# Performance work log

Measured on AMD Instinct MI355X. Metric: run time of the kernel, lower is better.

The kernel has to match this reference:

```python
import jax, jax.numpy as jnp
import numpy as np
import math

B, S, D, H = 4, 1024, 1024, 16
DK = D // H


def setup_inputs() -> dict:
    key = jax.random.key(0)
    ks = jax.random.split(key, 13)
    s = 1.0 / math.sqrt(D)
    inp = {
        "query": jax.random.normal(ks[0], (B, S, D), jnp.float32),
        "key": jax.random.normal(ks[1], (B, S, D), jnp.float32),
        "value": jax.random.normal(ks[2], (B, S, D), jnp.float32),
        "mask": jax.random.randint(ks[3], (B, S, S), 0, 2, jnp.int32),
        "wq": jax.random.normal(ks[4], (D, D), jnp.float32) * s,
        "bq": jax.random.normal(ks[5], (D,), jnp.float32) * s,
        "wk": jax.random.normal(ks[6], (D, D), jnp.float32) * s,
        "bk": jax.random.normal(ks[7], (D,), jnp.float32) * s,
        "wv": jax.random.normal(ks[8], (D, D), jnp.float32) * s,
        "bv": jax.random.normal(ks[9], (D,), jnp.float32) * s,
        "wo": jax.random.normal(ks[10], (D, D), jnp.float32) * s,
        "bo": jax.random.normal(ks[11], (D,), jnp.float32) * s,
    }
    return inp


def reference(query, key, value, mask, wq, bq, wk, bk, wv, bv, wo, bo):
    # QKV projections, split into heads: [B,S,D] -> [B,H,S,DK]
    def proj(x, w, b):
        return (x @ w.T + b).reshape(B, S, H, DK).transpose(0, 2, 1, 3)

    q = proj(query, wq, bq)
    k = proj(key, wk, bk)
    v = proj(value, wv, bv)

    scores = jnp.einsum("bhqd,bhkd->bhqk", q, k) / math.sqrt(DK)
    scores = scores + mask[:, None, :, :].astype(scores.dtype) * (-1e9)
    p = jax.nn.softmax(scores, axis=-1)
    x = jnp.einsum("bhqk,bhkd->bhqd", p, v)
    x = x.transpose(0, 2, 1, 3).reshape(B, S, D)
    # output projection (dropout is identity in eval)
    return x @ wo.T + bo
```

## Files before the change

### kernel.cpp

```cpp
#include <hip/hip_runtime.h>
#include <hip/hip_bf16.h>


typedef __bf16 bf16x8 __attribute__((ext_vector_type(8)));
typedef float f32x4 __attribute__((ext_vector_type(4)));
typedef unsigned short us8 __attribute__((ext_vector_type(8)));
typedef unsigned short us4 __attribute__((ext_vector_type(4)));

#define MFMA(a, b, c) __builtin_amdgcn_mfma_f32_16x16x32_bf16(a, b, c, 0, 0, 0)
#define EXP2(x) __builtin_amdgcn_exp2f(x)

__device__ __forceinline__ unsigned short f2b(float f) {
  return __builtin_bit_cast(unsigned short, __float2bfloat16(f));
}
__device__ __forceinline__ float b2f(unsigned short u) {
  return __builtin_bit_cast(float, (unsigned)u << 16);
}
__device__ __forceinline__ unsigned cvtpk(float lo, float hi) {
  unsigned r;
  asm("v_cvt_pk_bf16_f32 %0, %1, %2" : "=v"(r) : "v"(lo), "v"(hi));
  return r;
}
__device__ __forceinline__ bf16x8 ldbf8(const unsigned short* p) {
  return __builtin_bit_cast(bf16x8, *reinterpret_cast<const us8*>(p));
}
__device__ __forceinline__ us8 cvt8(float4 a, float4 b) {
  us8 o;
  o[0] = f2b(a.x); o[1] = f2b(a.y); o[2] = f2b(a.z); o[3] = f2b(a.w);
  o[4] = f2b(b.x); o[5] = f2b(b.y); o[6] = f2b(b.z); o[7] = f2b(b.w);
  return o;
}
__device__ __forceinline__ void glds16(const void* g, void* l) {
  __builtin_amdgcn_global_load_lds(
      (const __attribute__((address_space(1))) unsigned int*)g,
      (__attribute__((address_space(3))) unsigned int*)l, 16, 0, 0);
}

__global__ __launch_bounds__(256)
void prep(const float* __restrict__ query, const float* __restrict__ key,
          const float* __restrict__ value, const float* __restrict__ wq,
          const float* __restrict__ wk, const float* __restrict__ wv,
          unsigned short* __restrict__ Abfq, unsigned short* __restrict__ Abfk,
          unsigned short* __restrict__ Abfv, unsigned short* __restrict__ Wb) {
  const int bid = blockIdx.x, tid = threadIdx.x;
  const float* src;
  unsigned short* dst;
  size_t off;
  if (bid < 1536) {
    const int widx = bid >> 9;
    src = (widx == 0) ? wq : (widx == 1) ? wk : wv;
    dst = Wb + (size_t)widx * 1048576;
    off = (size_t)(bid & 511) * 2048 + tid * 8;
  } else if (bid < 3584) {
    src = query; dst = Abfq; off = (size_t)(bid - 1536) * 2048 + tid * 8;
  } else if (bid < 5632) {
    src = key; dst = Abfk; off = (size_t)(bid - 3584) * 2048 + tid * 8;
  } else {
    src = value; dst = Abfv; off = (size_t)(bid - 5632) * 2048 + tid * 8;
  }
  const float4* p = reinterpret_cast<const float4*>(src + off);
  *reinterpret_cast<us8*>(dst + off) = cvt8(p[0], p[1]);
}

__global__ __launch_bounds__(256)
void maskcvt(const int* __restrict__ mask, unsigned short* __restrict__ Mf) {
  const int idx = blockIdx.x * 256 + threadIdx.x;
  const int wl = idx & 63, tile = idx >> 6;
  const int kt = tile & 63, qt = (tile >> 6) & 63, b = tile >> 12;
  const int lr = wl & 15, lg = wl >> 4;
  const int4 mv = *reinterpret_cast<const int4*>(
      mask + (size_t)(b * 1024 + qt * 16 + lr) * 1024 + kt * 16 + lg * 4);
  us4 o;
  o[0] = mv.x ? 0xCEACu : 0xC1C0u;
  o[1] = mv.y ? 0xCEACu : 0xC1C0u;
  o[2] = mv.z ? 0xCEACu : 0xC1C0u;
  o[3] = mv.w ? 0xCEACu : 0xC1C0u;
  *reinterpret_cast<us4*>(Mf + (size_t)idx * 4) = o;
}

__global__ __launch_bounds__(256)
void cvt_w(const float* __restrict__ src, unsigned short* __restrict__ dst) {
  const size_t off = (size_t)blockIdx.x * 2048 + threadIdx.x * 8;
  const float4* p = reinterpret_cast<const float4*>(src + off);
  *reinterpret_cast<us8*>(dst + off) = cvt8(p[0], p[1]);
}

__global__ __launch_bounds__(256, 4)
void gemm_proj(const unsigned short* __restrict__ Aq,
               const unsigned short* __restrict__ Ak,
               const unsigned short* __restrict__ Av_bf,
               const float* __restrict__ Av_f32,
               const unsigned short* __restrict__ Wb,
               const float* __restrict__ bq, const float* __restrict__ bk,
               const float* __restrict__ bv, unsigned short* __restrict__ Qb,
               unsigned short* __restrict__ Kf, unsigned short* __restrict__ Vf,
               float qscale) {
  constexpr int K = 1024, N = 1024;
  __shared__ __align__(16) unsigned short As[2][128 * 32];
  __shared__ __align__(16) unsigned short Bs[2][128 * 32];
  const int lid = blockIdx.x + (blockIdx.y << 5) + (blockIdx.z << 8);
  const int xcd = lid & 7, slot = lid >> 3;
  const int chunk = ((slot >> 3) << 3) + xcd;
  const int z = chunk >> 5;
  const int bm = (chunk & 31) * 128;
  const int bn = (slot & 7) * 128;

  const unsigned short* Abf = (z == 0) ? Aq : (z == 1) ? Ak : Av_bf;
  const bool f32path = (z == 2) && (Av_bf == nullptr);
  const unsigned short* Bw = Wb + (size_t)z * 1048576;
  const float* bias = (z == 0) ? bq : (z == 1) ? bk : bv;
  const int t = threadIdx.x;
  const int w = t >> 6, lane = t & 63, lr = lane & 15, lg = lane >> 4;
  const int wr = w >> 1, wc = w & 1;

#define SWZ(row) ((((row) ^ ((row) >> 2)) & 3) << 4)

  f32x4 acc[4][4];
#pragma unroll
  for (int m = 0; m < 4; ++m)
#pragma unroll
    for (int n = 0; n < 4; ++n) acc[m][n] = f32x4{0.f, 0.f, 0.f, 0.f};

  auto stageA = [&](int k0, int buf) {
#pragma unroll
    for (int it = 0; it < 2; ++it) {
      const int s = it * 256 + t, row = s >> 2, cb = (s & 3) * 16;
      const char* g = (const char*)Abf + ((size_t)(bm + row) * 1024 + k0) * 2 +
                      (cb ^ SWZ(row));
      char* l = (char*)&As[buf][0] + (it * 256 + w * 64) * 16;
      glds16(g, l);
    }
  };
  auto stageB = [&](int k0, int buf) {
#pragma unroll
    for (int it = 0; it < 2; ++it) {
      const int s = it * 256 + t, row = s >> 2, cb = (s & 3) * 16;
      const char* g = (const char*)Bw + ((size_t)(bn + row) * 1024 + k0) * 2 +
                      (cb ^ SWZ(row));
      char* l = (char*)&Bs[buf][0] + (it * 256 + w * 64) * 16;
      glds16(g, l);
    }
  };
#define STA8(buf, it, v)                                                       \
  {                                                                            \
    const int s_ = (it) * 256 + t, row_ = s_ >> 2, cb_ = (s_ & 3) * 16;        \
    *reinterpret_cast<us8*>((char*)&As[buf][0] + row_ * 64 +                   \
                            (cb_ ^ SWZ(row_))) = (v);                          \
  }

  if (f32path) {
#pragma unroll
    for (int it = 0; it < 2; ++it) {
      const int s = it * 256 + t, row = s >> 2, col = (s & 3) * 8;
      const float4* p =
          reinterpret_cast<const float4*>(Av_f32 + (size_t)(bm + row) * K + col);
      STA8(0, it, cvt8(p[0], p[1]));
    }
  } else {
    stageA(0, 0);
  }
  stageB(0, 0);
  __syncthreads();

  for (int c = 0; c < 32; ++c) {
    const int buf = c & 1;
    float4 fa[4];
    if (c < 31) {
      const int k1 = (c + 1) * 32;
      if (f32path) {
#pragma unroll
        for (int it = 0; it < 2; ++it) {
          const int s = it * 256 + t, row = s >> 2, col = (s & 3) * 8;
          const float4* p = reinterpret_cast<const float4*>(
              Av_f32 + (size_t)(bm + row) * K + k1 + col);
          fa[2 * it] = p[0];
          fa[2 * it + 1] = p[1];
        }
      } else {
        stageA(k1, buf ^ 1);
      }
      stageB(k1, buf ^ 1);
    }
    {
      bf16x8 af[4], bfr[4];
#pragma unroll
      for (int m = 0; m < 4; ++m) {
        const int row = wr * 64 + m * 16 + lr;
        af[m] = ldbf8((const unsigned short*)((char*)&As[buf][0] + row * 64 +
                                              ((lg * 16) ^ SWZ(row))));
      }
#pragma unroll
      for (int n = 0; n < 4; ++n) {
        const int row = wc * 64 + n * 16 + lr;
        bfr[n] = ldbf8((const unsigned short*)((char*)&Bs[buf][0] + row * 64 +
                                               ((lg * 16) ^ SWZ(row))));
      }
#pragma unroll
      for (int m = 0; m < 4; ++m)
#pragma unroll
        for (int n = 0; n < 4; ++n) acc[m][n] = MFMA(af[m], bfr[n], acc[m][n]);
    }
    if (c < 31 && f32path) {
#pragma unroll
      for (int it = 0; it < 2; ++it) STA8(buf ^ 1, it, cvt8(fa[2 * it], fa[2 * it + 1]));
    }
    __syncthreads();
  }
#undef STA8
#undef SWZ

#pragma unroll
  for (int m = 0; m < 4; ++m) {
    const int mr = bm + wr * 64 + m * 16 + lg * 4;
#pragma unroll
    for (int nt = 0; nt < 4; ++nt) {
      const int n = bn + wc * 64 + nt * 16 + lr;
      const float bb = bias[n];
      if (z == 0) {
#pragma unroll
        for (int r = 0; r < 4; ++r)
          Qb[(size_t)(mr + r) * N + n] = f2b((acc[m][nt][r] + bb) * qscale);
      } else if (z == 1) {
        const int b2 = mr >> 10, s0 = mr & 1023, hh = n >> 6, dd = n & 63;
        const size_t base = (size_t)(b2 * 16 + hh) * 65536 + (size_t)(dd >> 5) * 32768 +
                            (size_t)(s0 >> 4) * 512 +
                            (size_t)((s0 & 15) | (((dd >> 3) & 3) << 4)) * 8 + (dd & 7);
#pragma unroll
        for (int r = 0; r < 4; ++r) Kf[base + r * 8] = f2b(acc[m][nt][r] + bb);
      } else {
        const int b2 = mr >> 10, s0 = mr & 1023, hh = n >> 6, dd = n & 63;
        const size_t base = (size_t)(b2 * 16 + hh) * 65536 + (size_t)(s0 >> 5) * 2048 +
                            (size_t)(dd >> 4) * 512 +
                            (size_t)((dd & 15) | (((s0 >> 3) & 3) << 4)) * 8 + (s0 & 7);
        us4 pk;
#pragma unroll
        for (int r = 0; r < 4; ++r) pk[r] = f2b(acc[m][nt][r] + bb);
        *reinterpret_cast<us4*>(&Vf[base]) = pk;
      }
    }
  }
}

__global__ __launch_bounds__(256)
void gemm_out(const unsigned short* __restrict__ A, const unsigned short* __restrict__ Bw,
              const float* __restrict__ bias, float* __restrict__ Out) {
  constexpr int K = 1024, N = 1024;
  __shared__ __align__(16) unsigned short As[2][128 * 64];
  __shared__ __align__(16) unsigned short Bs[2][64 * 64];
  const int lid = blockIdx.x + (blockIdx.y << 5);
  const int xcd = lid & 7, slot = lid >> 3;
  const int chunk = ((slot >> 5) << 3) + xcd;
  const int pos = slot & 31;
  const int bm = ((chunk << 1) + (pos >> 4)) * 128;
  const int bn = (pos & 15) * 64;
  const int t = threadIdx.x;
  const int w = t >> 6, lane = t & 63, lr = lane & 15, lg = lane >> 4;
  const int wr = w >> 1, wc = w & 1;
  const int swzc = (lr & 7) << 4;

  f32x4 acc[4][2];
#pragma unroll
  for (int m = 0; m < 4; ++m)
#pragma unroll
    for (int n = 0; n < 2; ++n) acc[m][n] = f32x4{0.f, 0.f, 0.f, 0.f};

  auto stageA = [&](int k0, int buf) {
#pragma unroll
    for (int it = 0; it < 4; ++it) {
      const int s = it * 256 + t, row = s >> 3, cb = (s & 7) * 16;
      const char* g = (const char*)A + ((size_t)(bm + row) * 1024 + k0) * 2 +
                      (cb ^ ((row & 7) << 4));
      char* l = (char*)&As[buf][0] + (it * 256 + w * 64) * 16;
      glds16(g, l);
    }
  };
  auto stageB = [&](int k0, int buf) {
#pragma unroll
    for (int it = 0; it < 2; ++it) {
      const int s = it * 256 + t, row = s >> 3, cb = (s & 7) * 16;
      const char* g = (const char*)Bw + ((size_t)(bn + row) * 1024 + k0) * 2 +
                      (cb ^ ((row & 7) << 4));
      char* l = (char*)&Bs[buf][0] + (it * 256 + w * 64) * 16;
      glds16(g, l);
    }
  };

  stageA(0, 0);
  stageB(0, 0);
  __syncthreads();

  for (int c = 0; c < 16; ++c) {
    const int buf = c & 1;
    if (c < 15) {
      const int k1 = (c + 1) * 64;
      stageA(k1, buf ^ 1);
      stageB(k1, buf ^ 1);
    }
#pragma unroll
    for (int h2 = 0; h2 < 2; ++h2) {
      bf16x8 af[4], bfr[2];
#pragma unroll
      for (int m = 0; m < 4; ++m) {
        const int row = wr * 64 + m * 16 + lr;
        af[m] = ldbf8((const unsigned short*)((char*)&As[buf][0] + row * 128 +
                                              ((h2 * 64 + lg * 16) ^ swzc)));
      }
#pragma unroll
      for (int n = 0; n < 2; ++n) {
        const int row = wc * 32 + n * 16 + lr;
        bfr[n] = ldbf8((const unsigned short*)((char*)&Bs[buf][0] + row * 128 +
                                               ((h2 * 64 + lg * 16) ^ swzc)));
      }
#pragma unroll
      for (int m = 0; m < 4; ++m)
#pragma unroll
        for (int n = 0; n < 2; ++n) acc[m][n] = MFMA(af[m], bfr[n], acc[m][n]);
    }
    __syncthreads();
  }

#pragma unroll
  for (int m = 0; m < 4; ++m) {
    const int mr = bm + wr * 64 + m * 16 + lg * 4;
#pragma unroll
    for (int nt = 0; nt < 2; ++nt) {
      const int n = bn + wc * 32 + nt * 16 + lr;
      const float bb = bias[n];
#pragma unroll
      for (int r = 0; r < 4; ++r) Out[(size_t)(mr + r) * N + n] = acc[m][nt][r] + bb;
    }
  }
}

__global__ __launch_bounds__(256)
void attn_v7(const unsigned short* __restrict__ Qb,
             const unsigned short* __restrict__ Kf,
             const unsigned short* __restrict__ Vf,
             const unsigned short* __restrict__ Mf,
             unsigned short* __restrict__ ctx) {
  __shared__ __align__(16) unsigned short S[2][8192];
  __shared__ __align__(16) unsigned short sP[4][16 * 64];
  const int lid = blockIdx.x + (blockIdx.y << 6);
  const int xcd = lid & 7, slot = lid >> 3;
  const int bh = ((slot >> 4) << 3) + xcd;
  const int qb = slot & 15;
  const int b = bh >> 4, h = bh & 15;
  const int t = threadIdx.x, w = t >> 6, wl = t & 63, lr = wl & 15, lg = wl >> 4;
  const int q0 = qb * 64 + w * 16;
  const int swz = (lr & 7) << 4;

  const unsigned short* qp = Qb + (size_t)(b * 1024 + q0 + lr) * 1024 + h * 64 + lg * 8;
  const bf16x8 bq0 = ldbf8(qp);
  const bf16x8 bq1 = ldbf8(qp + 32);

  const unsigned short* KfB = Kf + (size_t)bh * 65536;
  const unsigned short* VfB = Vf + (size_t)bh * 65536;
  const unsigned short* mfp = Mf + (size_t)((b * 64 + qb * 4 + w) * 64) * 256 + wl * 4;

  f32x4 O[4];
  float l_ = 0.f;
#pragma unroll
  for (int dt = 0; dt < 4; ++dt) O[dt] = f32x4{0.f, 0.f, 0.f, 0.f};
  unsigned short* sp = &sP[w][0];

  auto stage = [&](int kc, int buf) {
    const unsigned short* srcs[4] = {KfB + kc * 2048, KfB + 32768 + kc * 2048,
                                     VfB + kc * 4096, VfB + kc * 4096 + 2048};
#pragma unroll
    for (int r = 0; r < 4; ++r) {
      const char* g = (const char*)(srcs[r] + (size_t)t * 8);
      char* l = (char*)&S[buf][r * 2048 + w * 512];
      glds16(g, l);
    }
  };

  stage(0, 0);
  __syncthreads();

  for (int kc = 0; kc < 16; ++kc) {
    const int buf = kc & 1;
    if (kc < 15) stage(kc + 1, buf ^ 1);

    us4 mk[4];
#pragma unroll
    for (int t4 = 0; t4 < 4; ++t4)
      mk[t4] = *reinterpret_cast<const us4*>(mfp + (size_t)(kc * 4 + t4) * 256);

    bf16x8 ak[4][2];
#pragma unroll
    for (int t4 = 0; t4 < 4; ++t4) {
      ak[t4][0] = ldbf8(&S[buf][t4 * 512 + wl * 8]);
      ak[t4][1] = ldbf8(&S[buf][2048 + t4 * 512 + wl * 8]);
    }

    f32x4 sc[4];
    __builtin_amdgcn_s_setprio(1);
#pragma unroll
    for (int t4 = 0; t4 < 4; ++t4) {
      f32x4 a;
#pragma unroll
      for (int r = 0; r < 4; ++r) a[r] = b2f(mk[t4][r]);
      a = MFMA(ak[t4][0], bq0, a);
      a = MFMA(ak[t4][1], bq1, a);
      sc[t4] = a;
    }
    __builtin_amdgcn_s_setprio(0);

    float ps = 0.f;
#pragma unroll
    for (int t4 = 0; t4 < 4; ++t4) {
      const float e0 = EXP2(sc[t4][0]), e1 = EXP2(sc[t4][1]);
      const float e2 = EXP2(sc[t4][2]), e3 = EXP2(sc[t4][3]);
      ps += (e0 + e1) + (e2 + e3);
      uint2 pw;
      pw.x = cvtpk(e0, e1);
      pw.y = cvtpk(e2, e3);
      *reinterpret_cast<uint2*>((char*)sp + lr * 128 + ((t4 * 32 + lg * 8) ^ swz)) = pw;
    }
    ps += __shfl_xor(ps, 16);
    ps += __shfl_xor(ps, 32);
    l_ += ps;

    __builtin_amdgcn_s_setprio(1);
#pragma unroll
    for (int ks = 0; ks < 2; ++ks) {
      bf16x8 ap =
          ldbf8((const unsigned short*)((char*)sp + lr * 128 + ((ks * 64 + lg * 16) ^ swz)));
#pragma unroll
      for (int dt = 0; dt < 4; ++dt) {
        bf16x8 bv = ldbf8(&S[buf][4096 + ks * 2048 + dt * 512 + wl * 8]);
        O[dt] = MFMA(ap, bv, O[dt]);
      }
    }
    __builtin_amdgcn_s_setprio(0);

    __syncthreads();
  }

  float linv[4];
#pragma unroll
  for (int r = 0; r < 4; ++r) linv[r] = 1.0f / __shfl(l_, lg * 4 + r);
#pragma unroll
  for (int dt = 0; dt < 4; ++dt)
#pragma unroll
    for (int r = 0; r < 4; ++r)
      ctx[(size_t)(b * 1024 + q0 + lg * 4 + r) * 1024 + h * 64 + dt * 16 + lr] =
          f2b(O[dt][r] * linv[r]);
}

extern "C" void kernel_launch(void* const* d_in, const int* in_sizes, int n_in,
                              void* d_out, int out_size, void* d_ws, size_t ws_size,
                              hipStream_t stream) {
  const float* query = (const float*)d_in[0];
  const float* key   = (const float*)d_in[1];
  const float* value = (const float*)d_in[2];
  const int*   mask  = (const int*)d_in[3];
  const float* wq = (const float*)d_in[4];
  const float* bq = (const float*)d_in[5];
  const float* wk = (const float*)d_in[6];
  const float* bk = (const float*)d_in[7];
  const float* wv = (const float*)d_in[8];
  const float* bv = (const float*)d_in[9];
  const float* wo = (const float*)d_in[10];
  const float* bo = (const float*)d_in[11];
  float* out = (float*)d_out;

  const size_t SZ = (size_t)4096 * 1024;
  unsigned short* Qb   = (unsigned short*)d_ws;
  unsigned short* Kf   = Qb + SZ;
  unsigned short* Vf   = Kf + SZ;
  unsigned short* ctx  = Vf + SZ;
  unsigned short* Abfq = (unsigned short*)d_out;
  unsigned short* Wb   = Abfq + SZ;
  unsigned short* Mf   = (unsigned short*)d_out;
  unsigned short* Abfk = ctx;
  const bool big = ws_size >= (size_t)40 * 1024 * 1024;
  unsigned short* Abfv = big ? (ctx + SZ) : nullptr;
  unsigned short* Wob  = Vf;

  const float qscale = 0.125f * 1.4426950408889634f;
  dim3 blk(256);
  prep<<<big ? 7680 : 5632, blk, 0, stream>>>(query, key, value, wq, wk, wv,
                                              Abfq, Abfk, Abfv, Wb);
  gemm_proj<<<dim3(32, 8, 3), blk, 0, stream>>>(Abfq, Abfk, Abfv, value, Wb,
                                                bq, bk, bv, Qb, Kf, Vf, qscale);
  maskcvt<<<4096, blk, 0, stream>>>(mask, Mf);
  attn_v7<<<dim3(64, 16), blk, 0, stream>>>(Qb, Kf, Vf, Mf, ctx);
  cvt_w<<<512, blk, 0, stream>>>(wo, Wob);
  gemm_out<<<dim3(32, 16), blk, 0, stream>>>(ctx, Wob, bo, out);
}
```

Before: 116.5 us.

## Pre-tile bf16 operands into MFMA fragment layout and load directly to registers

The prep kernel now writes the bf16 inputs and weights in a tiled layout where each 16x32 MFMA fragment is a contiguous 512-element block. The projection GEMM drops its LDS staging and barriers and loads fragments straight from global memory into registers, double-buffered in registers. The occupancy hint in launch bounds is removed. This removes LDS traffic and synchronisation, but each wave now issues its own global loads with no sharing through LDS, so L2 traffic rises and there is more latency to hide.

New measurement: 129.4 us. +11.1%, slower.

```diff
diff --git a/kernel.cpp b/kernel.cpp
--- a/kernel.cpp
+++ b/kernel.cpp
@@ -35,6 +35,7 @@
       (const __attribute__((address_space(1))) unsigned int*)g,
       (__attribute__((address_space(3))) unsigned int*)l, 16, 0, 0);
 }
+
 
 __global__ __launch_bounds__(256)
 void prep(const float* __restrict__ query, const float* __restrict__ key,
@@ -59,7 +60,10 @@
     src = value; dst = Abfv; off = (size_t)(bid - 5632) * 2048 + tid * 8;
   }
   const float4* p = reinterpret_cast<const float4*>(src + off);
-  *reinterpret_cast<us8*>(dst + off) = cvt8(p[0], p[1]);
+  const int row = (int)(off >> 10), col = (int)(off & 1023);
+  const size_t daddr = ((size_t)((row >> 4) * 32 + (col >> 5)) << 9) +
+                       (size_t)(((row & 15) | (((col >> 3) & 3) << 4)) << 3);
+  *reinterpret_cast<us8*>(dst + daddr) = cvt8(p[0], p[1]);
 }
 
 __global__ __launch_bounds__(256)
@@ -85,7 +89,7 @@
   *reinterpret_cast<us8*>(dst + off) = cvt8(p[0], p[1]);
 }
 
-__global__ __launch_bounds__(256, 4)
+__global__ __launch_bounds__(256)
 void gemm_proj(const unsigned short* __restrict__ Aq,
                const unsigned short* __restrict__ Ak,
                const unsigned short* __restrict__ Av_bf,
@@ -95,9 +99,7 @@
                const float* __restrict__ bv, unsigned short* __restrict__ Qb,
                unsigned short* __restrict__ Kf, unsigned short* __restrict__ Vf,
                float qscale) {
-  constexpr int K = 1024, N = 1024;
-  __shared__ __align__(16) unsigned short As[2][128 * 32];
-  __shared__ __align__(16) unsigned short Bs[2][128 * 32];
+  constexpr int N = 1024;
   const int lid = blockIdx.x + (blockIdx.y << 5) + (blockIdx.z << 8);
   const int xcd = lid & 7, slot = lid >> 3;
   const int chunk = ((slot >> 3) << 3) + xcd;
@@ -105,15 +107,15 @@
   const int bm = (chunk & 31) * 128;
   const int bn = (slot & 7) * 128;
 
-  const unsigned short* Abf = (z == 0) ? Aq : (z == 1) ? Ak : Av_bf;
+  const unsigned short* AbfF = (z == 0) ? Aq : (z == 1) ? Ak : Av_bf;
   const bool f32path = (z == 2) && (Av_bf == nullptr);
-  const unsigned short* Bw = Wb + (size_t)z * 1048576;
+  const unsigned short* WbF = Wb + (size_t)z * 1048576;
   const float* bias = (z == 0) ? bq : (z == 1) ? bk : bv;
   const int t = threadIdx.x;
-  const int w = t >> 6, lane = t & 63, lr = lane & 15, lg = lane >> 4;
+  const int w = t >> 6, wl = t & 63, lr = wl & 15, lg = wl >> 4;
   const int wr = w >> 1, wc = w & 1;
-
-#define SWZ(row) ((((row) ^ ((row) >> 2)) & 3) << 4)
+  const int mtB = (bm >> 4) + wr * 4;
+  const int ntB = (bn >> 4) + wc * 4;
 
   f32x4 acc[4][4];
 #pragma unroll
@@ -121,93 +123,42 @@
 #pragma unroll
     for (int n = 0; n < 4; ++n) acc[m][n] = f32x4{0.f, 0.f, 0.f, 0.f};
 
-  auto stageA = [&](int k0, int buf) {
-#pragma unroll
-    for (int it = 0; it < 2; ++it) {
-      const int s = it * 256 + t, row = s >> 2, cb = (s & 3) * 16;
-      const char* g = (const char*)Abf + ((size_t)(bm + row) * 1024 + k0) * 2 +
-                      (cb ^ SWZ(row));
-      char* l = (char*)&As[buf][0] + (it * 256 + w * 64) * 16;
-      glds16(g, l);
+  auto loadA = [&](int m, int kt) -> bf16x8 {
+    if (!f32path) {
+      return ldbf8(AbfF + ((size_t)((mtB + m) * 32 + kt) << 9) + wl * 8);
+    } else {
+      const int row = bm + wr * 64 + m * 16 + lr;
+      const float4* p = reinterpret_cast<const float4*>(
+          Av_f32 + (size_t)row * 1024 + kt * 32 + lg * 8);
+      return __builtin_bit_cast(bf16x8, cvt8(p[0], p[1]));
     }
   };
-  auto stageB = [&](int k0, int buf) {
-#pragma unroll
-    for (int it = 0; it < 2; ++it) {
-      const int s = it * 256 + t, row = s >> 2, cb = (s & 3) * 16;
-      const char* g = (const char*)Bw + ((size_t)(bn + row) * 1024 + k0) * 2 +
-                      (cb ^ SWZ(row));
-      char* l = (char*)&Bs[buf][0] + (it * 256 + w * 64) * 16;
-      glds16(g, l);
-    }
+  auto loadB = [&](int n, int kt) -> bf16x8 {
+    return ldbf8(WbF + ((size_t)((ntB + n) * 32 + kt) << 9) + wl * 8);
   };
-#define STA8(buf, it, v)                                                       \
+
+#define LOADF(A_, B_, kt)                                                      \
   {                                                                            \
-    const int s_ = (it) * 256 + t, row_ = s_ >> 2, cb_ = (s_ & 3) * 16;        \
-    *reinterpret_cast<us8*>((char*)&As[buf][0] + row_ * 64 +                   \
-                            (cb_ ^ SWZ(row_))) = (v);                          \
-  }
-
-  if (f32path) {
-#pragma unroll
-    for (int it = 0; it < 2; ++it) {
-      const int s = it * 256 + t, row = s >> 2, col = (s & 3) * 8;
-      const float4* p =
-          reinterpret_cast<const float4*>(Av_f32 + (size_t)(bm + row) * K + col);
-      STA8(0, it, cvt8(p[0], p[1]));
-    }
-  } else {
-    stageA(0, 0);
-  }
-  stageB(0, 0);
-  __syncthreads();
-
-  for (int c = 0; c < 32; ++c) {
-    const int buf = c & 1;
-    float4 fa[4];
-    if (c < 31) {
-      const int k1 = (c + 1) * 32;
-      if (f32path) {
-#pragma unroll
-        for (int it = 0; it < 2; ++it) {
-          const int s = it * 256 + t, row = s >> 2, col = (s & 3) * 8;
-          const float4* p = reinterpret_cast<const float4*>(
-              Av_f32 + (size_t)(bm + row) * K + k1 + col);
-          fa[2 * it] = p[0];
-          fa[2 * it + 1] = p[1];
-        }
-      } else {
-        stageA(k1, buf ^ 1);
-      }
-      stageB(k1, buf ^ 1);
-    }
-    {
-      bf16x8 af[4], bfr[4];
-#pragma unroll
-      for (int m = 0; m < 4; ++m) {
-        const int row = wr * 64 + m * 16 + lr;
-        af[m] = ldbf8((const unsigned short*)((char*)&As[buf][0] + row * 64 +
-                                              ((lg * 16) ^ SWZ(row))));
-      }
-#pragma unroll
-      for (int n = 0; n < 4; ++n) {
-        const int row = wc * 64 + n * 16 + lr;
-        bfr[n] = ldbf8((const unsigned short*)((char*)&Bs[buf][0] + row * 64 +
-                                               ((lg * 16) ^ SWZ(row))));
-      }
-#pragma unroll
-      for (int m = 0; m < 4; ++m)
-#pragma unroll
-        for (int n = 0; n < 4; ++n) acc[m][n] = MFMA(af[m], bfr[n], acc[m][n]);
-    }
-    if (c < 31 && f32path) {
-#pragma unroll
-      for (int it = 0; it < 2; ++it) STA8(buf ^ 1, it, cvt8(fa[2 * it], fa[2 * it + 1]));
-    }
-    __syncthreads();
-  }
-#undef STA8
-#undef SWZ
+    _Pragma("unroll") for (int i = 0; i < 4; ++i) A_[i] = loadA(i, (kt));      \
+    _Pragma("unroll") for (int i = 0; i < 4; ++i) B_[i] = loadB(i, (kt));      \
+  }
+#define MMF(A_, B_)                                                            \
+  {                                                                            \
+    _Pragma("unroll") for (int m = 0; m < 4; ++m)                              \
+        _Pragma("unroll") for (int n = 0; n < 4; ++n)                          \
+        acc[m][n] = MFMA(A_[m], B_[n], acc[m][n]);                             \
+  }
+
+  bf16x8 a0[4], b0[4], a1[4], b1[4];
+  LOADF(a0, b0, 0)
+  for (int kt = 0; kt < 32; kt += 2) {
+    LOADF(a1, b1, kt + 1)
+    MMF(a0, b0)
+    if (kt + 2 < 32) LOADF(a0, b0, kt + 2)
+    MMF(a1, b1)
+  }
+#undef LOADF
+#undef MMF
 
 #pragma unroll
   for (int m = 0; m < 4; ++m) {
```
